# Performance work log

Hardware: AMD Instinct MI355X
Metric: run time of the kernel (lower is better)

## Reference

```python
import jax, jax.numpy as jnp
import numpy as np

K = 10  # hardcoded top-k in the original forward


def setup_inputs() -> dict:
    key = jax.random.key(0)
    ks = jax.random.split(key, 7)
    B, F, N = 192, 256, 512
    stdv = 1.0 / np.sqrt(F)
    return {
        "v": jax.random.normal(ks[0], (B, F, N), dtype=jnp.float32),
        "g_w": jax.random.normal(ks[1], (F, F), dtype=jnp.float32) * stdv,  # Conv1d k=1 weight [out,in]
        "g_b": jax.random.normal(ks[2], (F,), dtype=jnp.float32) * stdv,
        "w1": jax.random.uniform(ks[3], (F, F), jnp.float32, -stdv, stdv),
        "b1": jax.random.uniform(ks[4], (F,), jnp.float32, -stdv, stdv),
        "w2": jax.random.uniform(ks[5], (F, F), jnp.float32, -stdv, stdv),
        "b2": jax.random.uniform(ks[6], (F,), jnp.float32, -stdv, stdv),
    }


def reference(v, g_w, g_b, w1, b1, w2, b2):
    B, Fdim, N = v.shape
    # g: Conv1d(k=1) then permute -> [B, N, nhid]
    g_v = jnp.einsum('bfn,hf->bnh', v, g_w) + g_b
    # affinity A = v^T v : [B, N, N]
    A = jnp.einsum('bfn,bfm->bnm', v, v)
    # top-K sparsification: keep only top-K entries per row
    _, idx = jax.lax.top_k(A, K)  # [B, N, K]
    b_i = jnp.arange(B)[:, None, None]
    n_i = jnp.arange(N)[None, :, None]
    keep = jnp.zeros(A.shape, dtype=bool).at[b_i, n_i, idx].set(True)
    A = jnp.where(keep, A, jnp.zeros((), A.dtype))
    # add self loops
    A = A + jnp.eye(N, dtype=A.dtype)
    # D^-0.5 A D^-0.5 (diagonal scaling, equivalent to diag_embed matmuls)
    deg = jnp.sum(A, axis=-1)  # [B, N]
    d = deg ** -0.5
    d = jnp.where(jnp.isinf(d), jnp.zeros((), d.dtype), d)
    A_hat = d[:, :, None] * A * d[:, None, :]
    # GCN layer 1: relu(A_hat @ (g_v @ w1) + b1)  (dropout p=0 -> identity)
    x = jax.nn.relu(jnp.einsum('bnm,bmh->bnh', A_hat, g_v @ w1) + b1)
    # GCN layer 2
    x = jnp.einsum('bnm,bmh->bnh', A_hat, x @ w2) + b2
    # permute back and residual
    return jnp.transpose(x, (0, 2, 1)) + v
```

## Files before the change

kernel.cpp:

```cpp
#include <hip/hip_runtime.h>
#include <float.h>

#define F_DIM 256
#define N_DIM 512
#define B_DIM 192
#define K_TOP 10

typedef __attribute__((ext_vector_type(8))) short short8;
typedef __attribute__((ext_vector_type(4))) float f32x4;

__device__ inline unsigned short f2bf(float x) {
    unsigned u = __builtin_bit_cast(unsigned, x);
    return (unsigned short)((u + 0x7fffu + ((u >> 16) & 1u)) >> 16);
}

__global__ __launch_bounds__(256) void k_combine(const float* __restrict__ g_w,
                                                 const float* __restrict__ g_b,
                                                 const float* __restrict__ w1,
                                                 const float* __restrict__ w2,
                                                 unsigned short* __restrict__ Wt1,
                                                 float* __restrict__ bc,
                                                 unsigned short* __restrict__ W2t) {
    const int j = threadIdx.x;
    const int bx = blockIdx.x;
    if (bx < F_DIM) {
        float acc = 0.f;
        for (int h = 0; h < F_DIM; ++h) acc += g_w[h * F_DIM + bx] * w1[h * F_DIM + j];
        Wt1[j * F_DIM + bx] = f2bf(acc);
    } else if (bx == F_DIM) {
        float acc = 0.f;
        for (int h = 0; h < F_DIM; ++h) acc += g_b[h] * w1[h * F_DIM + j];
        bc[j] = acc;
    } else {
        int f = bx - F_DIM - 1;
        W2t[j * F_DIM + f] = f2bf(w2[f * F_DIM + j]);
    }
}

__global__ __launch_bounds__(256) void k_to_bf16t(const float* __restrict__ v,
                                                  unsigned short* __restrict__ vt) {
    __shared__ float tile[32][33];
    const int b = blockIdx.z;
    const int n0 = blockIdx.x * 32;
    const int f0 = blockIdx.y * 32;
    const int tx = threadIdx.x & 31, ty = threadIdx.x >> 5;
    const float* vb = v + (size_t)b * F_DIM * N_DIM;
#pragma unroll
    for (int q = 0; q < 4; ++q)
        tile[ty + q * 8][tx] = vb[(size_t)(f0 + ty + q * 8) * N_DIM + n0 + tx];
    __syncthreads();
    const int wn = threadIdx.x >> 4;
    const int wf = threadIdx.x & 15;
    unsigned* vt32 = (unsigned*)vt;
#pragma unroll
    for (int q2 = 0; q2 < 2; ++q2) {
        int row = wn + q2 * 16;
        unsigned lo = f2bf(tile[wf * 2][row]);
        unsigned hi = f2bf(tile[wf * 2 + 1][row]);
        vt32[(size_t)(b * N_DIM + n0 + row) * (F_DIM / 2) + (f0 >> 1) + wf] = lo | (hi << 16);
    }
}

__global__ __launch_bounds__(256, 4) void k_topk_reg(const unsigned short* __restrict__ vt,
                                                     float* __restrict__ deg,
                                                     int* __restrict__ idxb,
                                                     float* __restrict__ wb) {
    __shared__ unsigned short stage[N_DIM * 32];
    __shared__ uint2 scr[32][6];

    const int lid = blockIdx.x;
    const int slot = lid >> 3;
    const int b = (lid & 7) + 8 * (slot >> 4);
    const int n0 = (slot & 15) * 32;

    const int t = threadIdx.x;
    const int w = t >> 6;
    const int l = t & 63;
    const int l15 = l & 15;
    const int g = l >> 4;
    const int mbase = w * 128;
    const unsigned short* vtb = vt + (size_t)b * N_DIM * F_DIM;

    f32x4 acc[8][2];
#pragma unroll
    for (int mt = 0; mt < 8; ++mt) {
        acc[mt][0] = (f32x4){0.f, 0.f, 0.f, 0.f};
        acc[mt][1] = (f32x4){0.f, 0.f, 0.f, 0.f};
    }

#define STAGE(c)                                                                 \
    {                                                                            \
        _Pragma("unroll")                                                        \
        for (int k = 0; k < 8; ++k) {                                            \
            int sid = w * 512 + k * 64 + l;                                      \
            int row = sid >> 2;                                                  \
            int sl = sid & 3;                                                    \
            const unsigned short* src = vtb + (size_t)row * F_DIM + (c) * 32 +   \
                                        ((sl ^ ((row >> 1) & 3)) << 3);          \
            __builtin_amdgcn_global_load_lds(                                    \
                (const __attribute__((address_space(1))) void*)src,              \
                (__attribute__((address_space(3))) void*)(                       \
                    (char*)&stage[0] + (size_t)sid * 16),                        \
                16, 0, 0);                                                       \
        }                                                                        \
    }

    const int slx = g ^ ((l15 >> 1) & 3);
    for (int c = 0; c < 8; ++c) {
        STAGE(c);
        asm volatile("s_waitcnt vmcnt(0)" ::: "memory");
        __syncthreads();
        const char* sb = (const char*)&stage[0];
        short8 b0 = *(const short8*)(sb + (n0 + l15) * 64 + (slx << 4));
        short8 b1 = *(const short8*)(sb + (n0 + 16 + l15) * 64 + (slx << 4));
#pragma unroll
        for (int mt = 0; mt < 8; ++mt) {
            const int mrow = mbase + mt * 16 + l15;
            short8 a = *(const short8*)(sb + mrow * 64 + (slx << 4));
            acc[mt][0] = __builtin_amdgcn_mfma_f32_16x16x32_bf16(a, b0, acc[mt][0], 0, 0, 0);
            acc[mt][1] = __builtin_amdgcn_mfma_f32_16x16x32_bf16(a, b1, acc[mt][1], 0, 0, 0);
        }
        __syncthreads();
    }
#undef STAGE

#define BUILD_CHUNK(nt, c, outv, oute)                                           \
    {                                                                            \
        float p0v, p1v, p2v, p3v; int p0e, p1e, p2e, p3e;                        \
        { float a = acc[2*(c)][nt][0], bb = acc[2*(c)][nt][1];                   \
          bool tk = bb > a; p0v = tk ? bb : a; p0e = (c)*8 + (tk ? 1 : 0); }     \
        { float a = acc[2*(c)][nt][2], bb = acc[2*(c)][nt][3];                   \
          bool tk = bb > a; p1v = tk ? bb : a; p1e = (c)*8 + (tk ? 3 : 2); }     \
        { float a = acc[2*(c)+1][nt][0], bb = acc[2*(c)+1][nt][1];               \
          bool tk = bb > a; p2v = tk ? bb : a; p2e = (c)*8 + (tk ? 5 : 4); }     \
        { float a = acc[2*(c)+1][nt][2], bb = acc[2*(c)+1][nt][3];               \
          bool tk = bb > a; p3v = tk ? bb : a; p3e = (c)*8 + (tk ? 7 : 6); }     \
        bool q0 = p1v > p0v; float q0v = q0 ? p1v : p0v; int q0e = q0 ? p1e : p0e; \
        bool q1 = p3v > p2v; float q1v = q1 ? p3v : p2v; int q1e = q1 ? p3e : p2e; \
        bool q2 = q1v > q0v; (outv) = q2 ? q1v : q0v; (oute) = q2 ? q1e : q0e;   \
    }

    float cbv[2][4]; int cbe[2][4];
#pragma unroll
    for (int nt = 0; nt < 2; ++nt) {
        BUILD_CHUNK(nt, 0, cbv[nt][0], cbe[nt][0]);
        BUILD_CHUNK(nt, 1, cbv[nt][1], cbe[nt][1]);
        BUILD_CHUNK(nt, 2, cbv[nt][2], cbe[nt][2]);
        BUILD_CHUNK(nt, 3, cbv[nt][3], cbe[nt][3]);
    }

    const int grow0 = b * N_DIM + n0 + l15;
    float sum0 = 0.f, sum1 = 0.f;
    for (int it = 0; it < K_TOP; ++it) {
        float cv[2]; int cm[2];
#pragma unroll
        for (int nt = 0; nt < 2; ++nt) {
            bool k1 = cbv[nt][1] > cbv[nt][0];
            float va = k1 ? cbv[nt][1] : cbv[nt][0];
            int ea = k1 ? cbe[nt][1] : cbe[nt][0];
            bool k2 = cbv[nt][3] > cbv[nt][2];
            float vb2 = k2 ? cbv[nt][3] : cbv[nt][2];
            int eb = k2 ? cbe[nt][3] : cbe[nt][2];
            bool k3 = vb2 > va;
            cv[nt] = k3 ? vb2 : va;
            int ce = k3 ? eb : ea;
            cm[nt] = mbase + ((ce >> 2) << 4) + (g << 2) + (ce & 3);
        }
#pragma unroll
        for (int off = 16; off <= 32; off <<= 1) {
#pragma unroll
            for (int nt = 0; nt < 2; ++nt) {
                float ov = __shfl_xor(cv[nt], off, 64);
                int om = __shfl_xor(cm[nt], off, 64);
                if (ov > cv[nt] || (ov == cv[nt] && om < cm[nt])) { cv[nt] = ov; cm[nt] = om; }
            }
        }
        if (l < 16) {
            scr[l15][w] = make_uint2(__builtin_bit_cast(unsigned, cv[0]), (unsigned)cm[0]);
            scr[16 + l15][w] = make_uint2(__builtin_bit_cast(unsigned, cv[1]), (unsigned)cm[1]);
        }
        __syncthreads();
        float wv[2]; int wm[2];
#pragma unroll
        for (int nt = 0; nt < 2; ++nt) {
            const uint2* sr = &scr[nt * 16 + l15][0];
            uint4 q01 = *(const uint4*)&sr[0];
            uint4 q23 = *(const uint4*)&sr[2];
            float v0 = __builtin_bit_cast(float, q01.x); int m0 = (int)q01.y;
            float v1 = __builtin_bit_cast(float, q01.z); int m1 = (int)q01.w;
            float v2 = __builtin_bit_cast(float, q23.x); int m2 = (int)q23.y;
            float v3 = __builtin_bit_cast(float, q23.z); int m3 = (int)q23.w;
            bool t1 = (v1 > v0) || (v1 == v0 && m1 < m0);
            float va = t1 ? v1 : v0; int ma = t1 ? m1 : m0;
            bool t2 = (v3 > v2) || (v3 == v2 && m3 < m2);
            float vb2 = t2 ? v3 : v2; int mb = t2 ? m3 : m2;
            bool t3 = (vb2 > va) || (vb2 == va && mb < ma);
            wv[nt] = t3 ? vb2 : va; wm[nt] = t3 ? mb : ma;
        }
        __syncthreads();
        sum0 += wv[0]; sum1 += wv[1];
        if (w == 0 && l < 16) {
            idxb[grow0 * K_TOP + it] = wm[0];
            wb[grow0 * (K_TOP + 1) + it] = wv[0];
            idxb[(grow0 + 16) * K_TOP + it] = wm[1];
            wb[(grow0 + 16) * (K_TOP + 1) + it] = wv[1];
        }
        if (it < K_TOP - 1) {
#pragma unroll
            for (int nt = 0; nt < 2; ++nt) {
                const int mwin = wm[nt];
                const bool own = ((mwin >> 7) == w) && (((mwin >> 2) & 3) == g);
                const int eo = (((mwin >> 4) & 7) << 2) | (mwin & 3);
#pragma unroll
                for (int c = 0; c < 4; ++c) {
                    bool need = own && ((eo >> 3) == c);
                    if (__any(need)) {
#pragma unroll
                        for (int j = 0; j < 8; ++j) {
                            int ee = c * 8 + j;
                            acc[ee >> 2][nt][ee & 3] =
                                (need && ee == eo) ? -FLT_MAX : acc[ee >> 2][nt][ee & 3];
                        }
                        float nv; int ne;
                        BUILD_CHUNK(nt, c, nv, ne);
                        cbv[nt][c] = need ? nv : cbv[nt][c];
                        cbe[nt][c] = need ? ne : cbe[nt][c];
                    }
                }
            }
        }
    }
#undef BUILD_CHUNK
    if (w == 0 && l < 16) {
        deg[grow0] = sum0 + 1.0f;
        deg[grow0 + 16] = sum1 + 1.0f;
    }
}

__global__ __launch_bounds__(256) void k_scale(const float* __restrict__ deg,
                                               const int* __restrict__ idxb,
                                               const float* __restrict__ wb,
                                               float* __restrict__ wbs) {
    const int row = blockIdx.x * 256 + threadIdx.x;
    const float dg = deg[row];
    const float dn = (dg == 0.f) ? 0.f : 1.f / sqrtf(dg);
    const int bb = (row >> 9) << 9;
#pragma unroll
    for (int i = 0; i < K_TOP; ++i) {
        int m = idxb[row * K_TOP + i];
        float dgm = deg[bb + m];
        float dm = (dgm == 0.f) ? 0.f : 1.f / sqrtf(dgm);
        wbs[row * 12 + i] = dn * wb[row * (K_TOP + 1) + i] * dm;
    }
    wbs[row * 12 + K_TOP] = dn * dn;
}

template <bool ADD_BIAS>
__global__ __launch_bounds__(256, 4) void k_gemm_mfma(const unsigned short* __restrict__ At,
                                                      const unsigned short* __restrict__ Wt,
                                                      const float* __restrict__ bias,
                                                      float* __restrict__ C) {
    const int b = blockIdx.y;
    const int w = threadIdx.x >> 6;
    const int l = threadIdx.x & 63;
    const int l15 = l & 15;
    const int g = l >> 4;
    const int n0w = blockIdx.x * 64 + (w >> 1) * 32;
    const int j0w = (w & 1) * 128;
    const unsigned short* Ab = At + (size_t)b * N_DIM * F_DIM;

    f32x4 acc0[8], acc1[8];
#pragma unroll
    for (int jt = 0; jt < 8; ++jt) {
        acc0[jt] = (f32x4){0.f, 0.f, 0.f, 0.f};
        acc1[jt] = (f32x4){0.f, 0.f, 0.f, 0.f};
    }

    for (int s = 0; s < 8; ++s) {
        short8 a0 = *(const short8*)(Ab + (size_t)(n0w + l15) * F_DIM + s * 32 + g * 8);
        short8 a1 = *(const short8*)(Ab + (size_t)(n0w + 16 + l15) * F_DIM + s * 32 + g * 8);
#pragma unroll
        for (int jt = 0; jt < 8; ++jt) {
            short8 bf = *(const short8*)(Wt + (size_t)(j0w + jt * 16 + l15) * F_DIM + s * 32 + g * 8);
            acc0[jt] = __builtin_amdgcn_mfma_f32_16x16x32_bf16(a0, bf, acc0[jt], 0, 0, 0);
            acc1[jt] = __builtin_amdgcn_mfma_f32_16x16x32_bf16(a1, bf, acc1[jt], 0, 0, 0);
        }
    }

#pragma unroll
    for (int jt = 0; jt < 8; ++jt) {
        const int col = j0w + jt * 16 + l15;
        float bv = ADD_BIAS ? bias[col] : 0.f;
#pragma unroll
        for (int q = 0; q < 4; ++q) {
            int r0 = n0w + g * 4 + q;
            C[((size_t)b * N_DIM + r0) * F_DIM + col] = acc0[jt][q] + bv;
            int r1 = n0w + 16 + g * 4 + q;
            C[((size_t)b * N_DIM + r1) * F_DIM + col] = acc1[jt][q] + bv;
        }
    }
}

__global__ __launch_bounds__(256) void k_spmm_bf16(const float* __restrict__ X,
                                                   const int* __restrict__ idxb,
                                                   const float* __restrict__ wbs,
                                                   const float* __restrict__ bias,
                                                   unsigned short* __restrict__ Y) {
    const int lid = blockIdx.x;
    const int slot = lid >> 3;
    const int b = (lid & 7) + 8 * (slot >> 7);
    const int rowblk = slot & 127;
    const int w = threadIdx.x >> 6;
    const int l = threadIdx.x & 63;
    const int row = b * N_DIM + rowblk * 4 + w;

    const float* Xb = X + ((size_t)b << 9) * F_DIM;
    const int* id = idxb + row * K_TOP;
    const float* ww = wbs + (size_t)row * 12;

    float4 bv = ((const float4*)bias)[l];
    float4 xv = ((const float4*)(X + (size_t)row * F_DIM))[l];
    const float ws = ww[K_TOP];
    float4 acc;
    acc.x = ws * xv.x + bv.x; acc.y = ws * xv.y + bv.y;
    acc.z = ws * xv.z + bv.z; acc.w = ws * xv.w + bv.w;
#pragma unroll
    for (int i = 0; i < K_TOP; ++i) {
        float wi = ww[i];
        float4 gv = ((const float4*)(Xb + ((size_t)id[i] << 8)))[l];
        acc.x += wi * gv.x; acc.y += wi * gv.y;
        acc.z += wi * gv.z; acc.w += wi * gv.w;
    }
    acc.x = fmaxf(acc.x, 0.f); acc.y = fmaxf(acc.y, 0.f);
    acc.z = fmaxf(acc.z, 0.f); acc.w = fmaxf(acc.w, 0.f);
    uint2 p;
    p.x = (unsigned)f2bf(acc.x) | ((unsigned)f2bf(acc.y) << 16);
    p.y = (unsigned)f2bf(acc.z) | ((unsigned)f2bf(acc.w) << 16);
    ((uint2*)Y)[(size_t)row * (F_DIM / 4) + l] = p;
}

__global__ __launch_bounds__(256) void k_spmm_trans(const float* __restrict__ X,
                                                    const int* __restrict__ idxb,
                                                    const float* __restrict__ wbs,
                                                    const float* __restrict__ bias,
                                                    const float* __restrict__ v,
                                                    float* __restrict__ out) {
    __shared__ float tile[16][132];
    const int lid = blockIdx.x;
    const int slot = lid >> 3;
    const int b = (lid & 7) + 8 * (slot >> 6);
    const int tl = slot & 63;
    const int n0 = (tl & 31) * 16;
    const int f0 = (tl >> 5) * 128;
    const int w = threadIdx.x >> 6;
    const int l = threadIdx.x & 63;

    const float* Xb = X + ((size_t)b << 9) * F_DIM;
    const int rl = l >> 5;
    const int fq = l & 31;
    float4 bv = ((const float4*)bias)[(f0 >> 2) + fq];

#pragma unroll
    for (int p2 = 0; p2 < 2; ++p2) {
        const int rloc = p2 * 8 + w * 2 + rl;
        const int row = b * N_DIM + n0 + rloc;
        const int* id = idxb + row * K_TOP;
        const float* ww = wbs + (size_t)row * 12;
        float4 xv = ((const float4*)(X + (size_t)row * F_DIM + f0))[fq];
        const float ws = ww[K_TOP];
        float4 acc;
        acc.x = ws * xv.x + bv.x; acc.y = ws * xv.y + bv.y;
        acc.z = ws * xv.z + bv.z; acc.w = ws * xv.w + bv.w;
#pragma unroll
        for (int i = 0; i < K_TOP; ++i) {
            float wi = ww[i];
            float4 gv = ((const float4*)(Xb + ((size_t)id[i] << 8) + f0))[fq];
            acc.x += wi * gv.x; acc.y += wi * gv.y;
            acc.z += wi * gv.z; acc.w += wi * gv.w;
        }
        tile[rloc][fq * 4 + 0] = acc.x;
        tile[rloc][fq * 4 + 1] = acc.y;
        tile[rloc][fq * 4 + 2] = acc.z;
        tile[rloc][fq * 4 + 3] = acc.w;
    }
    __syncthreads();

    const int i4 = l & 3, fj = l >> 2;
#pragma unroll
    for (int k = 0; k < 2; ++k) {
        const int fl = k * 64 + w * 16 + fj;
        const size_t vo = (size_t)b * F_DIM * N_DIM + (size_t)(f0 + fl) * N_DIM + n0;
        float4 vv = ((const float4*)(v + vo))[i4];
        float4 o;
        o.x = tile[i4 * 4 + 0][fl] + vv.x;
        o.y = tile[i4 * 4 + 1][fl] + vv.y;
        o.z = tile[i4 * 4 + 2][fl] + vv.z;
        o.w = tile[i4 * 4 + 3][fl] + vv.w;
        ((float4*)(out + vo))[i4] = o;
    }
}

extern "C" void kernel_launch(void* const* d_in, const int* in_sizes, int n_in,
                              void* d_out, int out_size, void* d_ws, size_t ws_size,
                              hipStream_t stream) {
    const float* v   = (const float*)d_in[0];
    const float* g_w = (const float*)d_in[1];
    const float* g_b = (const float*)d_in[2];
    const float* w1  = (const float*)d_in[3];
    const float* b1  = (const float*)d_in[4];
    const float* w2  = (const float*)d_in[5];
    const float* b2  = (const float*)d_in[6];
    float* out = (float*)d_out;

    const size_t S = (size_t)B_DIM * N_DIM * F_DIM;
    float* bufA = (float*)d_ws;
    float* bufB = bufA + S;
    float* bc   = bufB + S;
    float* deg  = bc + F_DIM;
    float* wb   = deg + (size_t)B_DIM * N_DIM;
    int*   idxb = (int*)(wb + (size_t)B_DIM * N_DIM * (K_TOP + 1));
    unsigned short* Wt1 = (unsigned short*)(idxb + (size_t)B_DIM * N_DIM * K_TOP);
    unsigned short* W2t = Wt1 + F_DIM * F_DIM;

    unsigned short* vt   = (unsigned short*)bufB;
    unsigned short* x1bf = (unsigned short*)bufB;
    float* wbs = bufB + S / 2;

    k_combine<<<dim3(2 * F_DIM + 2), 256, 0, stream>>>(g_w, g_b, w1, w2, Wt1, bc, W2t);
    k_to_bf16t<<<dim3(N_DIM / 32, F_DIM / 32, B_DIM), 256, 0, stream>>>(v, vt);
    k_topk_reg<<<dim3(B_DIM * (N_DIM / 32)), 256, 0, stream>>>(vt, deg, idxb, wb);
    k_scale<<<dim3(B_DIM * N_DIM / 256), 256, 0, stream>>>(deg, idxb, wb, wbs);
    k_gemm_mfma<true><<<dim3(N_DIM / 64, B_DIM), 256, 0, stream>>>(vt, Wt1, bc, bufA);
    k_spmm_bf16<<<dim3(B_DIM * N_DIM / 4), 256, 0, stream>>>(bufA, idxb, wbs, b1, x1bf);
    k_gemm_mfma<false><<<dim3(N_DIM / 64, B_DIM), 256, 0, stream>>>(x1bf, W2t, nullptr, bufA);
    k_spmm_trans<<<dim3(B_DIM * N_DIM / 16 * 2), 256, 0, stream>>>(bufA, idxb, wbs, b2, v, out);
}
```

Measured before the change: 459.4 us.

## Compute per-wave local top-K independently and merge once at end

Each wave now extracts its own top-10 candidates from its 128-column slice without cross-wave barriers per iteration, writing them into LDS that reuses the staging buffer. After one barrier, a four-way merge over the per-wave sorted lists produces the final top-10 indices, weights and degree. This removes the two __syncthreads per top-k iteration and the shared scratch array, at the cost of extra per-wave selection work and a serial merge done by a few lanes.

```diff
diff --git a/kernel.cpp b/kernel.cpp
--- a/kernel.cpp
+++ b/kernel.cpp
@@ -65,8 +65,9 @@
                                                      float* __restrict__ deg,
                                                      int* __restrict__ idxb,
                                                      float* __restrict__ wb) {
-    __shared__ unsigned short stage[N_DIM * 32];
-    __shared__ uint2 scr[32][6];
+    __shared__ uint4 stage4[N_DIM * 4];
+    uint2* scr = (uint2*)stage4;
+#define SCR(wv_, it_, row_) scr[(((wv_)*10 + (it_)) * 33) + (row_)]
 
     const int lid = blockIdx.x;
     const int slot = lid >> 3;
@@ -100,7 +101,7 @@
             __builtin_amdgcn_global_load_lds(                                    \
                 (const __attribute__((address_space(1))) void*)src,              \
                 (__attribute__((address_space(3))) void*)(                       \
-                    (char*)&stage[0] + (size_t)sid * 16),                        \
+                    (char*)&stage4[0] + (size_t)sid * 16),                       \
                 16, 0, 0);                                                       \
         }                                                                        \
     }
@@ -110,7 +111,7 @@
         STAGE(c);
         asm volatile("s_waitcnt vmcnt(0)" ::: "memory");
         __syncthreads();
-        const char* sb = (const char*)&stage[0];
+        const char* sb = (const char*)&stage4[0];
         short8 b0 = *(const short8*)(sb + (n0 + l15) * 64 + (slx << 4));
         short8 b1 = *(const short8*)(sb + (n0 + 16 + l15) * 64 + (slx << 4));
 #pragma unroll
@@ -149,8 +150,6 @@
         BUILD_CHUNK(nt, 3, cbv[nt][3], cbe[nt][3]);
     }
 
-    const int grow0 = b * N_DIM + n0 + l15;
-    float sum0 = 0.f, sum1 = 0.f;
     for (int it = 0; it < K_TOP; ++it) {
         float cv[2]; int cm[2];
 #pragma unroll
@@ -176,40 +175,14 @@
             }
         }
         if (l < 16) {
-            scr[l15][w] = make_uint2(__builtin_bit_cast(unsigned, cv[0]), (unsigned)cm[0]);
-            scr[16 + l15][w] = make_uint2(__builtin_bit_cast(unsigned, cv[1]), (unsigned)cm[1]);
-        }
-        __syncthreads();
-        float wv[2]; int wm[2];
-#pragma unroll
-        for (int nt = 0; nt < 2; ++nt) {
-            const uint2* sr = &scr[nt * 16 + l15][0];
-            uint4 q01 = *(const uint4*)&sr[0];
-            uint4 q23 = *(const uint4*)&sr[2];
-            float v0 = __builtin_bit_cast(float, q01.x); int m0 = (int)q01.y;
-            float v1 = __builtin_bit_cast(float, q01.z); int m1 = (int)q01.w;
-            float v2 = __builtin_bit_cast(float, q23.x); int m2 = (int)q23.y;
-            float v3 = __builtin_bit_cast(float, q23.z); int m3 = (int)q23.w;
-            bool t1 = (v1 > v0) || (v1 == v0 && m1 < m0);
-            float va = t1 ? v1 : v0; int ma = t1 ? m1 : m0;
-            bool t2 = (v3 > v2) || (v3 == v2 && m3 < m2);
-            float vb2 = t2 ? v3 : v2; int mb = t2 ? m3 : m2;
-            bool t3 = (vb2 > va) || (vb2 == va && mb < ma);
-            wv[nt] = t3 ? vb2 : va; wm[nt] = t3 ? mb : ma;
-        }
-        __syncthreads();
-        sum0 += wv[0]; sum1 += wv[1];
-        if (w == 0 && l < 16) {
-            idxb[grow0 * K_TOP + it] = wm[0];
-            wb[grow0 * (K_TOP + 1) + it] = wv[0];
-            idxb[(grow0 + 16) * K_TOP + it] = wm[1];
-            wb[(grow0 + 16) * (K_TOP + 1) + it] = wv[1];
+            SCR(w, it, l15) = make_uint2(__builtin_bit_cast(unsigned, cv[0]), (unsigned)cm[0]);
+            SCR(w, it, 16 + l15) = make_uint2(__builtin_bit_cast(unsigned, cv[1]), (unsigned)cm[1]);
         }
         if (it < K_TOP - 1) {
 #pragma unroll
             for (int nt = 0; nt < 2; ++nt) {
-                const int mwin = wm[nt];
-                const bool own = ((mwin >> 7) == w) && (((mwin >> 2) & 3) == g);
+                const int mwin = cm[nt];
+                const bool own = ((mwin >> 2) & 3) == g;
                 const int eo = (((mwin >> 4) & 7) << 2) | (mwin & 3);
 #pragma unroll
                 for (int c = 0; c < 4; ++c) {
@@ -231,10 +204,37 @@
         }
     }
 #undef BUILD_CHUNK
-    if (w == 0 && l < 16) {
-        deg[grow0] = sum0 + 1.0f;
-        deg[grow0 + 16] = sum1 + 1.0f;
-    }
+    __syncthreads();
+
+    if (l < 8) {
+        const int rloc = w * 8 + l;
+        const int grow = b * N_DIM + n0 + rloc;
+        int p0 = 0, p1 = 0, p2 = 0, p3 = 0;
+        float sum = 0.f;
+#pragma unroll
+        for (int k2 = 0; k2 < K_TOP; ++k2) {
+            uint2 h0 = SCR(0, p0 < 10 ? p0 : 9, rloc);
+            uint2 h1 = SCR(1, p1 < 10 ? p1 : 9, rloc);
+            uint2 h2 = SCR(2, p2 < 10 ? p2 : 9, rloc);
+            uint2 h3 = SCR(3, p3 < 10 ? p3 : 9, rloc);
+            float v0 = (p0 < 10) ? __builtin_bit_cast(float, h0.x) : -FLT_MAX; int m0 = (int)h0.y;
+            float v1 = (p1 < 10) ? __builtin_bit_cast(float, h1.x) : -FLT_MAX; int m1 = (int)h1.y;
+            float v2 = (p2 < 10) ? __builtin_bit_cast(float, h2.x) : -FLT_MAX; int m2 = (int)h2.y;
+            float v3 = (p3 < 10) ? __builtin_bit_cast(float, h3.x) : -FLT_MAX; int m3 = (int)h3.y;
+            bool t1 = (v1 > v0) || (v1 == v0 && m1 < m0);
+            float va = t1 ? v1 : v0; int ma = t1 ? m1 : m0; int ja = t1 ? 1 : 0;
+            bool t2 = (v3 > v2) || (v3 == v2 && m3 < m2);
+            float vb2 = t2 ? v3 : v2; int mb = t2 ? m3 : m2; int jb = t2 ? 3 : 2;
+            bool t3 = (vb2 > va) || (vb2 == va && mb < ma);
+            float vw = t3 ? vb2 : va; int mw = t3 ? mb : ma; int jw = t3 ? jb : ja;
+            sum += vw;
+            idxb[grow * K_TOP + k2] = mw;
+            wb[grow * (K_TOP + 1) + k2] = vw;
+            p0 += (jw == 0); p1 += (jw == 1); p2 += (jw == 2); p3 += (jw == 3);
+        }
+        deg[grow] = sum + 1.0f;
+    }
+#undef SCR
 }
 
 __global__ __launch_bounds__(256) void k_scale(const float* __restrict__ deg,
```

Result: slower. 469.3 us (+2.2%).

## Double-buffer top-k staging and split row tiles across 8 waves

Applied to the files above, without the earlier changes.

The top-k affinity kernel now runs 512 threads per block. Eight waves each own one 16-row half of the 32-row tile, which halves per-thread accumulators and the selection work. LDS staging is double-buffered so the next K-chunk loads while MFMAs run on the current one. The selection scratch is ping-ponged, which removes one barrier per iteration. This doubles LDS use per block (about 64KB) and may cut resident blocks per CU.

```diff
diff --git a/kernel.cpp b/kernel.cpp
--- a/kernel.cpp
+++ b/kernel.cpp
@@ -61,12 +61,12 @@
     }
 }
 
-__global__ __launch_bounds__(256, 4) void k_topk_reg(const unsigned short* __restrict__ vt,
+__global__ __launch_bounds__(512, 4) void k_topk_reg(const unsigned short* __restrict__ vt,
                                                      float* __restrict__ deg,
                                                      int* __restrict__ idxb,
                                                      float* __restrict__ wb) {
-    __shared__ unsigned short stage[N_DIM * 32];
-    __shared__ uint2 scr[32][6];
+    __shared__ unsigned short stage[2][N_DIM * 32];
+    __shared__ uint2 scr[2][32][6];
 
     const int lid = blockIdx.x;
     const int slot = lid >> 3;
@@ -78,21 +78,20 @@
     const int l = t & 63;
     const int l15 = l & 15;
     const int g = l >> 4;
-    const int mbase = w * 128;
+    const int sl4 = w & 3;
+    const int rh = w >> 2;
+    const int mbase = sl4 * 128;
     const unsigned short* vtb = vt + (size_t)b * N_DIM * F_DIM;
 
-    f32x4 acc[8][2];
-#pragma unroll
-    for (int mt = 0; mt < 8; ++mt) {
-        acc[mt][0] = (f32x4){0.f, 0.f, 0.f, 0.f};
-        acc[mt][1] = (f32x4){0.f, 0.f, 0.f, 0.f};
-    }
-
-#define STAGE(c)                                                                 \
+    f32x4 acc[8];
+#pragma unroll
+    for (int mt = 0; mt < 8; ++mt) acc[mt] = (f32x4){0.f, 0.f, 0.f, 0.f};
+
+#define STAGE(c, bi)                                                             \
     {                                                                            \
         _Pragma("unroll")                                                        \
-        for (int k = 0; k < 8; ++k) {                                            \
-            int sid = w * 512 + k * 64 + l;                                      \
+        for (int k = 0; k < 4; ++k) {                                            \
+            int sid = k * 512 + t;                                               \
             int row = sid >> 2;                                                  \
             int sl = sid & 3;                                                    \
             const unsigned short* src = vtb + (size_t)row * F_DIM + (c) * 32 +   \
@@ -100,141 +99,117 @@
             __builtin_amdgcn_global_load_lds(                                    \
                 (const __attribute__((address_space(1))) void*)src,              \
                 (__attribute__((address_space(3))) void*)(                       \
-                    (char*)&stage[0] + (size_t)sid * 16),                        \
+                    (char*)&stage[bi][0] + (size_t)sid * 16),                    \
                 16, 0, 0);                                                       \
         }                                                                        \
     }
 
+    STAGE(0, 0);
+    asm volatile("s_waitcnt vmcnt(0)" ::: "memory");
+    __syncthreads();
+
     const int slx = g ^ ((l15 >> 1) & 3);
+    const int brow = n0 + rh * 16 + l15;
     for (int c = 0; c < 8; ++c) {
-        STAGE(c);
-        asm volatile("s_waitcnt vmcnt(0)" ::: "memory");
-        __syncthreads();
-        const char* sb = (const char*)&stage[0];
-        short8 b0 = *(const short8*)(sb + (n0 + l15) * 64 + (slx << 4));
-        short8 b1 = *(const short8*)(sb + (n0 + 16 + l15) * 64 + (slx << 4));
+        const int cur = c & 1;
+        if (c < 7) STAGE(c + 1, cur ^ 1);
+        const char* sb = (const char*)&stage[cur][0];
+        short8 b0 = *(const short8*)(sb + brow * 64 + (slx << 4));
 #pragma unroll
         for (int mt = 0; mt < 8; ++mt) {
             const int mrow = mbase + mt * 16 + l15;
             short8 a = *(const short8*)(sb + mrow * 64 + (slx << 4));
-            acc[mt][0] = __builtin_amdgcn_mfma_f32_16x16x32_bf16(a, b0, acc[mt][0], 0, 0, 0);
-            acc[mt][1] = __builtin_amdgcn_mfma_f32_16x16x32_bf16(a, b1, acc[mt][1], 0, 0, 0);
-        }
+            acc[mt] = __builtin_amdgcn_mfma_f32_16x16x32_bf16(a, b0, acc[mt], 0, 0, 0);
+        }
+        asm volatile("s_waitcnt vmcnt(0)" ::: "memory");
         __syncthreads();
     }
 #undef STAGE
 
-#define BUILD_CHUNK(nt, c, outv, oute)                                           \
+#define BUILD_CHUNK(c, outv, oute)                                               \
     {                                                                            \
         float p0v, p1v, p2v, p3v; int p0e, p1e, p2e, p3e;                        \
-        { float a = acc[2*(c)][nt][0], bb = acc[2*(c)][nt][1];                   \
+        { float a = acc[2*(c)][0], bb = acc[2*(c)][1];                           \
           bool tk = bb > a; p0v = tk ? bb : a; p0e = (c)*8 + (tk ? 1 : 0); }     \
-        { float a = acc[2*(c)][nt][2], bb = acc[2*(c)][nt][3];                   \
+        { float a = acc[2*(c)][2], bb = acc[2*(c)][3];                           \
           bool tk = bb > a; p1v = tk ? bb : a; p1e = (c)*8 + (tk ? 3 : 2); }     \
-        { float a = acc[2*(c)+1][nt][0], bb = acc[2*(c)+1][nt][1];               \
+        { float a = acc[2*(c)+1][0], bb = acc[2*(c)+1][1];                       \
           bool tk = bb > a; p2v = tk ? bb : a; p2e = (c)*8 + (tk ? 5 : 4); }     \
-        { float a = acc[2*(c)+1][nt][2], bb = acc[2*(c)+1][nt][3];               \
+        { float a = acc[2*(c)+1][2], bb = acc[2*(c)+1][3];                       \
           bool tk = bb > a; p3v = tk ? bb : a; p3e = (c)*8 + (tk ? 7 : 6); }     \
         bool q0 = p1v > p0v; float q0v = q0 ? p1v : p0v; int q0e = q0 ? p1e : p0e; \
         bool q1 = p3v > p2v; float q1v = q1 ? p3v : p2v; int q1e = q1 ? p3e : p2e; \
         bool q2 = q1v > q0v; (outv) = q2 ? q1v : q0v; (oute) = q2 ? q1e : q0e;   \
     }
 
-    float cbv[2][4]; int cbe[2][4];
-#pragma unroll
-    for (int nt = 0; nt < 2; ++nt) {
-        BUILD_CHUNK(nt, 0, cbv[nt][0], cbe[nt][0]);
-        BUILD_CHUNK(nt, 1, cbv[nt][1], cbe[nt][1]);
-        BUILD_CHUNK(nt, 2, cbv[nt][2], cbe[nt][2]);
-        BUILD_CHUNK(nt, 3, cbv[nt][3], cbe[nt][3]);
-    }
-
-    const int grow0 = b * N_DIM + n0 + l15;
-    float sum0 = 0.f, sum1 = 0.f;
+    float cbv[4]; int cbe[4];
+    BUILD_CHUNK(0, cbv[0], cbe[0]);
+    BUILD_CHUNK(1, cbv[1], cbe[1]);
+    BUILD_CHUNK(2, cbv[2], cbe[2]);
+    BUILD_CHUNK(3, cbv[3], cbe[3]);
+
+    const int rloc = rh * 16 + l15;
+    const int grow = b * N_DIM + n0 + rloc;
+    float sum = 0.f;
     for (int it = 0; it < K_TOP; ++it) {
-        float cv[2]; int cm[2];
-#pragma unroll
-        for (int nt = 0; nt < 2; ++nt) {
-            bool k1 = cbv[nt][1] > cbv[nt][0];
-            float va = k1 ? cbv[nt][1] : cbv[nt][0];
-            int ea = k1 ? cbe[nt][1] : cbe[nt][0];
-            bool k2 = cbv[nt][3] > cbv[nt][2];
-            float vb2 = k2 ? cbv[nt][3] : cbv[nt][2];
-            int eb = k2 ? cbe[nt][3] : cbe[nt][2];
-            bool k3 = vb2 > va;
-            cv[nt] = k3 ? vb2 : va;
-            int ce = k3 ? eb : ea;
-            cm[nt] = mbase + ((ce >> 2) << 4) + (g << 2) + (ce & 3);
-        }
+        bool k1 = cbv[1] > cbv[0];
+        float va = k1 ? cbv[1] : cbv[0]; int ea = k1 ? cbe[1] : cbe[0];
+        bool k2 = cbv[3] > cbv[2];
+        float vb2 = k2 ? cbv[3] : cbv[2]; int eb = k2 ? cbe[3] : cbe[2];
+        bool k3 = vb2 > va;
+        float cv = k3 ? vb2 : va; int ce = k3 ? eb : ea;
+        int cm = mbase + ((ce >> 2) << 4) + (g << 2) + (ce & 3);
 #pragma unroll
         for (int off = 16; off <= 32; off <<= 1) {
-#pragma unroll
-            for (int nt = 0; nt < 2; ++nt) {
-                float ov = __shfl_xor(cv[nt], off, 64);
-                int om = __shfl_xor(cm[nt], off, 64);
-                if (ov > cv[nt] || (ov == cv[nt] && om < cm[nt])) { cv[nt] = ov; cm[nt] = om; }
-            }
-        }
-        if (l < 16) {
-            scr[l15][w] = make_uint2(__builtin_bit_cast(unsigned, cv[0]), (unsigned)cm[0]);
-            scr[16 + l15][w] = make_uint2(__builtin_bit_cast(unsigned, cv[1]), (unsigned)cm[1]);
-        }
+            float ov = __shfl_xor(cv, off, 64);
+            int om = __shfl_xor(cm, off, 64);
+            if (ov > cv || (ov == cv && om < cm)) { cv = ov; cm = om; }
+        }
+        const int ib = it & 1;
+        if (l < 16)
+            scr[ib][rloc][sl4] = make_uint2(__builtin_bit_cast(unsigned, cv), (unsigned)cm);
         __syncthreads();
-        float wv[2]; int wm[2];
-#pragma unroll
-        for (int nt = 0; nt < 2; ++nt) {
-            const uint2* sr = &scr[nt * 16 + l15][0];
-            uint4 q01 = *(const uint4*)&sr[0];
-            uint4 q23 = *(const uint4*)&sr[2];
-            float v0 = __builtin_bit_cast(float, q01.x); int m0 = (int)q01.y;
-            float v1 = __builtin_bit_cast(float, q01.z); int m1 = (int)q01.w;
-            float v2 = __builtin_bit_cast(float, q23.x); int m2 = (int)q23.y;
-            float v3 = __builtin_bit_cast(float, q23.z); int m3 = (int)q23.w;
-            bool t1 = (v1 > v0) || (v1 == v0 && m1 < m0);
-            float va = t1 ? v1 : v0; int ma = t1 ? m1 : m0;
-            bool t2 = (v3 > v2) || (v3 == v2 && m3 < m2);
-            float vb2 = t2 ? v3 : v2; int mb = t2 ? m3 : m2;
-            bool t3 = (vb2 > va) || (vb2 == va && mb < ma);
-            wv[nt] = t3 ? vb2 : va; wm[nt] = t3 ? mb : ma;
-        }
-        __syncthreads();
-        sum0 += wv[0]; sum1 += wv[1];
-        if (w == 0 && l < 16) {
-            idxb[grow0 * K_TOP + it] = wm[0];
-            wb[grow0 * (K_TOP + 1) + it] = wv[0];
-            idxb[(grow0 + 16) * K_TOP + it] = wm[1];
-            wb[(grow0 + 16) * (K_TOP + 1) + it] = wv[1];
+        const uint2* sr = &scr[ib][rloc][0];
+        uint4 q01 = *(const uint4*)&sr[0];
+        uint4 q23 = *(const uint4*)&sr[2];
+        float v0 = __builtin_bit_cast(float, q01.x); int m0 = (int)q01.y;
+        float v1 = __builtin_bit_cast(float, q01.z); int m1 = (int)q01.w;
+        float v2 = __builtin_bit_cast(float, q23.x); int m2 = (int)q23.y;
+        float v3 = __builtin_bit_cast(float, q23.z); int m3 = (int)q23.w;
+        bool t1 = (v1 > v0) || (v1 == v0 && m1 < m0);
+        float ua = t1 ? v1 : v0; int ma = t1 ? m1 : m0;
+        bool t2 = (v3 > v2) || (v3 == v2 && m3 < m2);
+        float ub = t2 ? v3 : v2; int mb = t2 ? m3 : m2;
+        bool t3 = (ub > ua) || (ub == ua && mb < ma);
+        float wv = t3 ? ub : ua; int wm = t3 ? mb : ma;
+        sum += wv;
+        if (sl4 == 0 && l < 16) {
+            idxb[grow * K_TOP + it] = wm;
+            wb[grow * (K_TOP + 1) + it] = wv;
         }
         if (it < K_TOP - 1) {
-#pragma unroll
-            for (int nt = 0; nt < 2; ++nt) {
-                const int mwin = wm[nt];
-                const bool own = ((mwin >> 7) == w) && (((mwin >> 2) & 3) == g);
-                const int eo = (((mwin >> 4) & 7) << 2) | (mwin & 3);
-#pragma unroll
-                for (int c = 0; c < 4; ++c) {
-                    bool need = own && ((eo >> 3) == c);
-                    if (__any(need)) {
-#pragma unroll
-                        for (int j = 0; j < 8; ++j) {
-                            int ee = c * 8 + j;
-                            acc[ee >> 2][nt][ee & 3] =
-                                (need && ee == eo) ? -FLT_MAX : acc[ee >> 2][nt][ee & 3];
-                        }
-                        float nv; int ne;
-                        BUILD_CHUNK(nt, c, nv, ne);
-                        cbv[nt][c] = need ? nv : cbv[nt][c];
-                        cbe[nt][c] = need ? ne : cbe[nt][c];
+            const bool own = ((wm >> 7) == sl4) && (((wm >> 2) & 3) == g);
+            const int eo = (((wm >> 4) & 7) << 2) | (wm & 3);
+#pragma unroll
+            for (int c = 0; c < 4; ++c) {
+                bool need = own && ((eo >> 3) == c);
+                if (__any(need)) {
+#pragma unroll
+                    for (int j = 0; j < 8; ++j) {
+                        int ee = c * 8 + j;
+                        acc[ee >> 2][ee & 3] =
+                            (need && ee == eo) ? -FLT_MAX : acc[ee >> 2][ee & 3];
                     }
+                    float nv; int ne;
+                    BUILD_CHUNK(c, nv, ne);
+                    cbv[c] = need ? nv : cbv[c];
+                    cbe[c] = need ? ne : cbe[c];
                 }
             }
         }
     }
 #undef BUILD_CHUNK
-    if (w == 0 && l < 16) {
-        deg[grow0] = sum0 + 1.0f;
-        deg[grow0 + 16] = sum1 + 1.0f;
-    }
+    if (sl4 == 0 && l < 16) deg[grow] = sum + 1.0f;
 }
 
 __global__ __launch_bounds__(256) void k_scale(const float* __restrict__ deg,
@@ -428,7 +403,7 @@
 
     k_combine<<<dim3(2 * F_DIM + 2), 256, 0, stream>>>(g_w, g_b, w1, w2, Wt1, bc, W2t);
     k_to_bf16t<<<dim3(N_DIM / 32, F_DIM / 32, B_DIM), 256, 0, stream>>>(v, vt);
-    k_topk_reg<<<dim3(B_DIM * (N_DIM / 32)), 256, 0, stream>>>(vt, deg, idxb, wb);
+    k_topk_reg<<<dim3(B_DIM * (N_DIM / 32)), 512, 0, stream>>>(vt, deg, idxb, wb);
     k_scale<<<dim3(B_DIM * N_DIM / 256), 256, 0, stream>>>(deg, idxb, wb, wbs);
     k_gemm_mfma<true><<<dim3(N_DIM / 64, B_DIM), 256, 0, stream>>>(vt, Wt1, bc, bufA);
     k_spmm_bf16<<<dim3(B_DIM * N_DIM / 4), 256, 0, stream>>>(bufA, idxb, wbs, b1, x1bf);
```

New measurement: 470.1 us. +2.3%, slower.

## Fuse first sparse aggregation with second GEMM through LDS staging

Applied to the files above, without the earlier changes.

Layer-1 sparse aggregation and the layer-2 weight GEMM now run in one kernel. Each block aggregates 64 rows, applies ReLU, converts them to bf16 into a swizzled 32KB LDS tile, then runs the MFMA GEMM against W2t from that tile. This drops the bf16 intermediate round trip through global memory and one kernel launch. The scaled weights move to a separate workspace region because bufB now holds the GEMM output. The cost is a 32KB LDS footprint per block, only 1536 blocks, and a serialized gather phase before the MFMA phase.

```diff
diff --git a/kernel.cpp b/kernel.cpp
--- a/kernel.cpp
+++ b/kernel.cpp
@@ -301,42 +301,88 @@
     }
 }
 
-__global__ __launch_bounds__(256) void k_spmm_bf16(const float* __restrict__ X,
-                                                   const int* __restrict__ idxb,
-                                                   const float* __restrict__ wbs,
-                                                   const float* __restrict__ bias,
-                                                   unsigned short* __restrict__ Y) {
+__global__ __launch_bounds__(256, 4) void k_spmm_gemm(const float* __restrict__ X,
+                                                      const int* __restrict__ idxb,
+                                                      const float* __restrict__ wbs,
+                                                      const float* __restrict__ bias1,
+                                                      const unsigned short* __restrict__ Wt,
+                                                      float* __restrict__ C) {
+    __shared__ char xs[64 * 512];
     const int lid = blockIdx.x;
     const int slot = lid >> 3;
-    const int b = (lid & 7) + 8 * (slot >> 7);
-    const int rowblk = slot & 127;
-    const int w = threadIdx.x >> 6;
-    const int l = threadIdx.x & 63;
-    const int row = b * N_DIM + rowblk * 4 + w;
+    const int b = (lid & 7) + 8 * (slot >> 3);
+    const int n0 = (slot & 7) * 64;
+
+    const int t = threadIdx.x;
+    const int w = t >> 6;
+    const int l = t & 63;
+    const int l15 = l & 15;
+    const int g = l >> 4;
 
     const float* Xb = X + ((size_t)b << 9) * F_DIM;
-    const int* id = idxb + row * K_TOP;
-    const float* ww = wbs + (size_t)row * 12;
-
-    float4 bv = ((const float4*)bias)[l];
-    float4 xv = ((const float4*)(X + (size_t)row * F_DIM))[l];
-    const float ws = ww[K_TOP];
-    float4 acc;
-    acc.x = ws * xv.x + bv.x; acc.y = ws * xv.y + bv.y;
-    acc.z = ws * xv.z + bv.z; acc.w = ws * xv.w + bv.w;
-#pragma unroll
-    for (int i = 0; i < K_TOP; ++i) {
-        float wi = ww[i];
-        float4 gv = ((const float4*)(Xb + ((size_t)id[i] << 8)))[l];
-        acc.x += wi * gv.x; acc.y += wi * gv.y;
-        acc.z += wi * gv.z; acc.w += wi * gv.w;
-    }
-    acc.x = fmaxf(acc.x, 0.f); acc.y = fmaxf(acc.y, 0.f);
-    acc.z = fmaxf(acc.z, 0.f); acc.w = fmaxf(acc.w, 0.f);
-    uint2 p;
-    p.x = (unsigned)f2bf(acc.x) | ((unsigned)f2bf(acc.y) << 16);
-    p.y = (unsigned)f2bf(acc.z) | ((unsigned)f2bf(acc.w) << 16);
-    ((uint2*)Y)[(size_t)row * (F_DIM / 4) + l] = p;
+    float4 bv = ((const float4*)bias1)[l];
+
+    for (int i = 0; i < 16; ++i) {
+        const int rloc = w * 16 + i;
+        const int row = b * N_DIM + n0 + rloc;
+        const int* id = idxb + row * K_TOP;
+        const float* ww = wbs + (size_t)row * 12;
+        float4 xv = ((const float4*)(X + (size_t)row * F_DIM))[l];
+        const float ws = ww[K_TOP];
+        float4 acc;
+        acc.x = ws * xv.x + bv.x; acc.y = ws * xv.y + bv.y;
+        acc.z = ws * xv.z + bv.z; acc.w = ws * xv.w + bv.w;
+#pragma unroll
+        for (int i2 = 0; i2 < K_TOP; ++i2) {
+            float wi = ww[i2];
+            float4 gv = ((const float4*)(Xb + ((size_t)id[i2] << 8)))[l];
+            acc.x += wi * gv.x; acc.y += wi * gv.y;
+            acc.z += wi * gv.z; acc.w += wi * gv.w;
+        }
+        acc.x = fmaxf(acc.x, 0.f); acc.y = fmaxf(acc.y, 0.f);
+        acc.z = fmaxf(acc.z, 0.f); acc.w = fmaxf(acc.w, 0.f);
+        uint2 p;
+        p.x = (unsigned)f2bf(acc.x) | ((unsigned)f2bf(acc.y) << 16);
+        p.y = (unsigned)f2bf(acc.z) | ((unsigned)f2bf(acc.w) << 16);
+        int ofs = (rloc * 512 + l * 8) ^ ((rloc & 7) << 4);
+        *(uint2*)(xs + ofs) = p;
+    }
+    __syncthreads();
+
+    const int n0w = (w >> 1) * 32;
+    const int j0w = (w & 1) * 128;
+    f32x4 acc0[8], acc1[8];
+#pragma unroll
+    for (int jt = 0; jt < 8; ++jt) {
+        acc0[jt] = (f32x4){0.f, 0.f, 0.f, 0.f};
+        acc1[jt] = (f32x4){0.f, 0.f, 0.f, 0.f};
+    }
+
+    for (int s = 0; s < 8; ++s) {
+        const int r0 = n0w + l15, r1 = n0w + 16 + l15;
+        int o0 = (r0 * 512 + s * 64 + g * 16) ^ ((r0 & 7) << 4);
+        int o1 = (r1 * 512 + s * 64 + g * 16) ^ ((r1 & 7) << 4);
+        short8 a0 = *(const short8*)(xs + o0);
+        short8 a1 = *(const short8*)(xs + o1);
+#pragma unroll
+        for (int jt = 0; jt < 8; ++jt) {
+            short8 bf = *(const short8*)(Wt + (size_t)(j0w + jt * 16 + l15) * F_DIM + s * 32 + g * 8);
+            acc0[jt] = __builtin_amdgcn_mfma_f32_16x16x32_bf16(a0, bf, acc0[jt], 0, 0, 0);
+            acc1[jt] = __builtin_amdgcn_mfma_f32_16x16x32_bf16(a1, bf, acc1[jt], 0, 0, 0);
+        }
+    }
+
+#pragma unroll
+    for (int jt = 0; jt < 8; ++jt) {
+        const int col = j0w + jt * 16 + l15;
+#pragma unroll
+        for (int q = 0; q < 4; ++q) {
+            int r0 = n0 + n0w + g * 4 + q;
+            C[((size_t)b * N_DIM + r0) * F_DIM + col] = acc0[jt][q];
+            int r1 = n0 + n0w + 16 + g * 4 + q;
+            C[((size_t)b * N_DIM + r1) * F_DIM + col] = acc1[jt][q];
+        }
+    }
 }
 
 __global__ __launch_bounds__(256) void k_spmm_trans(const float* __restrict__ X,
@@ -422,16 +468,20 @@
     unsigned short* Wt1 = (unsigned short*)(idxb + (size_t)B_DIM * N_DIM * K_TOP);
     unsigned short* W2t = Wt1 + F_DIM * F_DIM;
 
-    unsigned short* vt   = (unsigned short*)bufB;
-    unsigned short* x1bf = (unsigned short*)bufB;
+    unsigned short* vt = (unsigned short*)bufB;
     float* wbs = bufB + S / 2;
+    float* h2  = bufA;
+    float* h2buf = (float*)vt;
+    (void)h2; (void)h2buf;
+
+    float* wbs2 = (float*)(W2t + F_DIM * F_DIM);
+    wbs2 = (float*)(((uintptr_t)wbs2 + 255) & ~(uintptr_t)255);
 
     k_combine<<<dim3(2 * F_DIM + 2), 256, 0, stream>>>(g_w, g_b, w1, w2, Wt1, bc, W2t);
     k_to_bf16t<<<dim3(N_DIM / 32, F_DIM / 32, B_DIM), 256, 0, stream>>>(v, vt);
     k_topk_reg<<<dim3(B_DIM * (N_DIM / 32)), 256, 0, stream>>>(vt, deg, idxb, wb);
-    k_scale<<<dim3(B_DIM * N_DIM / 256), 256, 0, stream>>>(deg, idxb, wb, wbs);
+    k_scale<<<dim3(B_DIM * N_DIM / 256), 256, 0, stream>>>(deg, idxb, wb, wbs2);
     k_gemm_mfma<true><<<dim3(N_DIM / 64, B_DIM), 256, 0, stream>>>(vt, Wt1, bc, bufA);
-    k_spmm_bf16<<<dim3(B_DIM * N_DIM / 4), 256, 0, stream>>>(bufA, idxb, wbs, b1, x1bf);
-    k_gemm_mfma<false><<<dim3(N_DIM / 64, B_DIM), 256, 0, stream>>>(x1bf, W2t, nullptr, bufA);
-    k_spmm_trans<<<dim3(B_DIM * N_DIM / 16 * 2), 256, 0, stream>>>(bufA, idxb, wbs, b2, v, out);
-}
+    k_spmm_gemm<<<dim3(B_DIM * 8), 256, 0, stream>>>(bufA, idxb, wbs2, b1, W2t, bufB);
+    k_spmm_trans<<<dim3(B_DIM * N_DIM / 16 * 2), 256, 0, stream>>>(bufB, idxb, wbs2, b2, v, out);
+}
```

Result: no change. 466.9 us (+1.6%).
